# Performance work log

Measured on AMD Instinct MI355X. Metric: run time of the kernel, lower is better.

The kernel has to match this reference:

```python
import jax, jax.numpy as jnp
import numpy as np


def setup_inputs() -> dict:
    key = jax.random.key(0)
    k1, k2, k3 = jax.random.split(key, 3)
    n_nodes, d = 1_000_000, 128
    B, L, w, neg_size = 1024, 80, 5, 4
    A = L - w + 1  # 76 anchors per walk
    walk = jax.random.randint(k1, (B, L), 0, n_nodes)
    # torch.randint(low=1, high=n_nodes-1) -> values in [1, n_nodes-2]
    neg = jax.random.randint(k2, (B, A, neg_size), 1, n_nodes - 1)
    embed = jax.random.normal(k3, (n_nodes, d), dtype=jnp.float32)
    return {"walk": walk, "neg": neg, "embed": embed}


def reference(walk, neg, embed):
    B, L = walk.shape
    A = neg.shape[1]          # L - window_size + 1
    w = L - A + 1             # window_size
    anc = walk[:, :A]                                       # [B, A]
    # pos[b, t, i] = walk[b, t + 1 + i], i in [0, w-2]
    sl = jnp.arange(A)[:, None] + jnp.arange(1, w)[None, :]  # [A, w-1]
    pos = walk[:, sl]                                        # [B, A, w-1]
    e_anc = embed[anc]                                       # [B, A, D]
    # fused gather + per-window dot products
    pos_logit = jnp.einsum('bacd,bad->bac', embed[pos], e_anc)  # [B, A, w-1]
    neg_logit = jnp.einsum('bacd,bad->bac', embed[neg], e_anc)  # [B, A, neg]
    # BCEWithLogitsLoss with labels 1 (pos) and 0 (neg), mean over all elements:
    #   label=1 -> softplus(-x);  label=0 -> softplus(x)
    total = pos_logit.size + neg_logit.size
    loss = (jnp.sum(jax.nn.softplus(-pos_logit)) +
            jnp.sum(jax.nn.softplus(neg_logit))) / total
    return loss
```

## Files before the change

### kernel.cpp

```cpp
#include <hip/hip_runtime.h>
#include <math.h>

#define BD   1024
#define LW   80
#define AA   76
#define NEGS 4
#define D    128
#define PAIRS (BD * AA)
#define WAVES_PER_BLOCK 4
#define PAIRS_PER_WAVE 19
#define NBLOCKS BD

__device__ __forceinline__ float softplus(float x) {
    return fmaxf(x, 0.0f) + log1pf(__expf(-fabsf(x)));
}

__global__ __launch_bounds__(256, 4) void sg_partial(
    const int* __restrict__ walk, const int* __restrict__ neg,
    const float* __restrict__ embed, float* __restrict__ ws)
{
    __shared__ float s_wsum[WAVES_PER_BLOCK];
    const int tid  = threadIdx.x;
    const int lane = tid & 63;
    const int wave = __builtin_amdgcn_readfirstlane(tid >> 6);
    const int b    = blockIdx.x;
    const int a0   = wave * PAIRS_PER_WAVE;

    const float* erow = embed + (size_t)(lane * 2);
    const int*   wrow = walk + b * LW + a0;
    const int*   nrow = neg + (size_t)(b * AA + a0) * NEGS;

    float2 r[5];
    #pragma unroll
    for (int j = 0; j < 5; ++j)
        r[j] = *(const float2*)(erow + (size_t)wrow[j] * D);

    const bool hi1 = lane & 1;
    const bool hi2 = lane & 2;
    const bool hi3 = lane & 4;

    float wsum = 0.0f;

    #pragma unroll
    for (int i = 0; i < PAIRS_PER_WAVE; ++i) {
        const int4 nv = *(const int4*)(nrow + i * NEGS);
        const float2 e4 = *(const float2*)(erow + (size_t)nv.x * D);
        const float2 e5 = *(const float2*)(erow + (size_t)nv.y * D);
        const float2 e6 = *(const float2*)(erow + (size_t)nv.z * D);
        const float2 e7 = *(const float2*)(erow + (size_t)nv.w * D);

        const float2 ea = r[0];
        float a0v = fmaf(ea.x, r[1].x, ea.y * r[1].y);
        float a1v = fmaf(ea.x, r[2].x, ea.y * r[2].y);
        float a2v = fmaf(ea.x, r[3].x, ea.y * r[3].y);
        float a3v = fmaf(ea.x, r[4].x, ea.y * r[4].y);
        float a4v = fmaf(ea.x, e4.x,  ea.y * e4.y);
        float a5v = fmaf(ea.x, e5.x,  ea.y * e5.y);
        float a6v = fmaf(ea.x, e6.x,  ea.y * e6.y);
        float a7v = fmaf(ea.x, e7.x,  ea.y * e7.y);

        float b0 = (hi1 ? a4v : a0v) + __shfl_xor(hi1 ? a0v : a4v, 1);
        float b1 = (hi1 ? a5v : a1v) + __shfl_xor(hi1 ? a1v : a5v, 1);
        float b2 = (hi1 ? a6v : a2v) + __shfl_xor(hi1 ? a2v : a6v, 1);
        float b3 = (hi1 ? a7v : a3v) + __shfl_xor(hi1 ? a3v : a7v, 1);

        float c0 = (hi2 ? b2 : b0) + __shfl_xor(hi2 ? b0 : b2, 2);
        float c1 = (hi2 ? b3 : b1) + __shfl_xor(hi2 ? b1 : b3, 2);

        float dv = (hi3 ? c1 : c0) + __shfl_xor(hi3 ? c0 : c1, 4);
        dv += __shfl_xor(dv, 8);
        dv += __shfl_xor(dv, 16);
        dv += __shfl_xor(dv, 32);
        wsum += softplus(hi1 ? dv : -dv);

        if (i < PAIRS_PER_WAVE - 1) {
            #pragma unroll
            for (int j = 0; j < 4; ++j) r[j] = r[j + 1];
            r[4] = *(const float2*)(erow + (size_t)wrow[i + 5] * D);
        }
    }

    #pragma unroll
    for (int m = 1; m < 64; m <<= 1) wsum += __shfl_xor(wsum, m);

    if (lane == 0) s_wsum[wave] = wsum * 0.125f;
    __syncthreads();
    if (tid == 0)
        ws[blockIdx.x] = s_wsum[0] + s_wsum[1] + s_wsum[2] + s_wsum[3];
}

__global__ __launch_bounds__(256) void sg_reduce(
    const float* __restrict__ ws, float* __restrict__ out)
{
    __shared__ float s[4];
    const int tid = threadIdx.x;
    float sum = 0.0f;
    #pragma unroll
    for (int i = 0; i < NBLOCKS / 256; ++i) sum += ws[tid + i * 256];
    #pragma unroll
    for (int m = 1; m < 64; m <<= 1) sum += __shfl_xor(sum, m);
    const int wave = tid >> 6;
    const int lane = tid & 63;
    if (lane == 0) s[wave] = sum;
    __syncthreads();
    if (tid == 0) {
        const float total = (float)((size_t)PAIRS * 8);
        out[0] = (s[0] + s[1] + s[2] + s[3]) * (1.0f / total);
    }
}

extern "C" void kernel_launch(void* const* d_in, const int* in_sizes, int n_in,
                              void* d_out, int out_size, void* d_ws, size_t ws_size,
                              hipStream_t stream) {
    const int*   walk  = (const int*)d_in[0];
    const int*   neg   = (const int*)d_in[1];
    const float* embed = (const float*)d_in[2];
    float* ws  = (float*)d_ws;
    float* out = (float*)d_out;

    sg_partial<<<NBLOCKS, 256, 0, stream>>>(walk, neg, embed, ws);
    sg_reduce<<<1, 256, 0, stream>>>(ws, out);
}
```

Before: 587.4 us.

## Process two anchor pairs per wave with half-wave float4 row loads

Each half of the wave now handles a different anchor pair, with each lane loading float4 (16 bytes) instead of float2. This halves the number of gather instructions per row and removes the final cross-half shuffle from the dot-product reduction. The loop now runs nine double steps plus a tail for the odd 19th pair, and next-step rows are prefetched one iteration ahead. The cost is extra select and swap shuffles to give each half its anchor vector, more register pressure, and a duplicated tail path whose scaling must stay correct.

```diff
diff --git a/kernel.cpp b/kernel.cpp
--- a/kernel.cpp
+++ b/kernel.cpp
@@ -15,6 +15,29 @@
     return fmaxf(x, 0.0f) + log1pf(__expf(-fabsf(x)));
 }
 
+__device__ __forceinline__ float dot4(float4 a, float4 b) {
+    return fmaf(a.x, b.x, fmaf(a.y, b.y, fmaf(a.z, b.z, a.w * b.w)));
+}
+
+__device__ __forceinline__ float4 sel4(bool c, float4 a, float4 b) {
+    float4 r;
+    r.x = c ? a.x : b.x;  r.y = c ? a.y : b.y;
+    r.z = c ? a.z : b.z;  r.w = c ? a.w : b.w;
+    return r;
+}
+
+__device__ __forceinline__ float4 swap32(float4 v) {
+    float4 r;
+    r.x = __shfl_xor(v.x, 32);  r.y = __shfl_xor(v.y, 32);
+    r.z = __shfl_xor(v.z, 32);  r.w = __shfl_xor(v.w, 32);
+    return r;
+}
+
+__device__ __forceinline__ float4 pload(const float* ebase, bool half, int i0, int i1) {
+    const int idx = half ? i1 : i0;
+    return *(const float4*)(ebase + (size_t)idx * D);
+}
+
 __global__ __launch_bounds__(256, 4) void sg_partial(
     const int* __restrict__ walk, const int* __restrict__ neg,
     const float* __restrict__ embed, float* __restrict__ ws)
@@ -22,42 +45,68 @@
     __shared__ float s_wsum[WAVES_PER_BLOCK];
     const int tid  = threadIdx.x;
     const int lane = tid & 63;
+    const int l32  = lane & 31;
+    const bool half = lane >= 32;
     const int wave = __builtin_amdgcn_readfirstlane(tid >> 6);
     const int b    = blockIdx.x;
     const int a0   = wave * PAIRS_PER_WAVE;
 
-    const float* erow = embed + (size_t)(lane * 2);
-    const int*   wrow = walk + b * LW + a0;
-    const int*   nrow = neg + (size_t)(b * AA + a0) * NEGS;
+    const float* ebase = embed + l32 * 4;
+    const int*   wrow  = walk + b * LW + a0;
+    const int*   nrow  = neg + (size_t)(b * AA + a0) * NEGS;
 
-    float2 r[5];
-    #pragma unroll
-    for (int j = 0; j < 5; ++j)
-        r[j] = *(const float2*)(erow + (size_t)wrow[j] * D);
+    float4 w01 = pload(ebase, half, wrow[0], wrow[1]);
+    float4 w23 = pload(ebase, half, wrow[2], wrow[3]);
+    float4 w45 = pload(ebase, half, wrow[4], wrow[5]);
+
+    int4 nva = *(const int4*)(nrow);
+    int4 nvb = *(const int4*)(nrow + 4);
+    float4 n01 = pload(ebase, half, nva.x, nva.y);
+    float4 n23 = pload(ebase, half, nva.z, nva.w);
+    float4 n45 = pload(ebase, half, nvb.x, nvb.y);
+    float4 n67 = pload(ebase, half, nvb.z, nvb.w);
 
     const bool hi1 = lane & 1;
     const bool hi2 = lane & 2;
     const bool hi3 = lane & 4;
 
     float wsum = 0.0f;
+    float tsum = 0.0f;
 
     #pragma unroll
-    for (int i = 0; i < PAIRS_PER_WAVE; ++i) {
-        const int4 nv = *(const int4*)(nrow + i * NEGS);
-        const float2 e4 = *(const float2*)(erow + (size_t)nv.x * D);
-        const float2 e5 = *(const float2*)(erow + (size_t)nv.y * D);
-        const float2 e6 = *(const float2*)(erow + (size_t)nv.z * D);
-        const float2 e7 = *(const float2*)(erow + (size_t)nv.w * D);
+    for (int d = 0; d < 9; ++d) {
+        float4 nw, m01, m23, m45, m67;
+        if (d < 8) {
+            nw = pload(ebase, half, wrow[2*d + 6], wrow[2*d + 7]);
+            const int4 pa = *(const int4*)(nrow + 8*(d + 1));
+            const int4 pb = *(const int4*)(nrow + 8*(d + 1) + 4);
+            m01 = pload(ebase, half, pa.x, pa.y);
+            m23 = pload(ebase, half, pa.z, pa.w);
+            m45 = pload(ebase, half, pb.x, pb.y);
+            m67 = pload(ebase, half, pb.z, pb.w);
+        } else {
+            const int i22 = wrow[22];
+            nw = pload(ebase, half, i22, i22);
+            const int4 pa = *(const int4*)(nrow + 72);
+            m01 = pload(ebase, half, pa.x, pa.y);
+            m23 = pload(ebase, half, pa.z, pa.w);
+            m45 = m01;  m67 = m23;
+        }
 
-        const float2 ea = r[0];
-        float a0v = fmaf(ea.x, r[1].x, ea.y * r[1].y);
-        float a1v = fmaf(ea.x, r[2].x, ea.y * r[2].y);
-        float a2v = fmaf(ea.x, r[3].x, ea.y * r[3].y);
-        float a3v = fmaf(ea.x, r[4].x, ea.y * r[4].y);
-        float a4v = fmaf(ea.x, e4.x,  ea.y * e4.y);
-        float a5v = fmaf(ea.x, e5.x,  ea.y * e5.y);
-        float a6v = fmaf(ea.x, e6.x,  ea.y * e6.y);
-        float a7v = fmaf(ea.x, e7.x,  ea.y * e7.y);
+        const float4 Y   = swap32(w01);
+        const float4 Z0  = sel4(half, Y, w01);
+        const float4 Z1  = sel4(half, w01, Y);
+        const float4 Aop = sel4(half, w01, w23);
+        const float4 Bop = sel4(half, w23, w45);
+
+        const float a0v = dot4(Z0, Aop);
+        const float a1v = dot4(Z0, Bop);
+        const float a2v = dot4(Z1, w23);
+        const float a3v = dot4(Z1, w45);
+        const float a4v = dot4(Z0, n01);
+        const float a5v = dot4(Z0, n23);
+        const float a6v = dot4(Z1, n45);
+        const float a7v = dot4(Z1, n67);
 
         float b0 = (hi1 ? a4v : a0v) + __shfl_xor(hi1 ? a0v : a4v, 1);
         float b1 = (hi1 ? a5v : a1v) + __shfl_xor(hi1 ? a1v : a5v, 1);
@@ -70,20 +119,37 @@
         float dv = (hi3 ? c1 : c0) + __shfl_xor(hi3 ? c0 : c1, 4);
         dv += __shfl_xor(dv, 8);
         dv += __shfl_xor(dv, 16);
-        dv += __shfl_xor(dv, 32);
         wsum += softplus(hi1 ? dv : -dv);
 
-        if (i < PAIRS_PER_WAVE - 1) {
-            #pragma unroll
-            for (int j = 0; j < 4; ++j) r[j] = r[j + 1];
-            r[4] = *(const float2*)(erow + (size_t)wrow[i + 5] * D);
-        }
+        w01 = w23;  w23 = w45;  w45 = nw;
+        n01 = m01;  n23 = m23;  n45 = m45;  n67 = m67;
     }
 
+    {
+        const float4 Y   = swap32(w01);
+        const float4 Z0  = sel4(half, Y, w01);
+        const float4 Aop = sel4(half, w01, w23);
+        const float4 Bop = sel4(half, w23, w45);
+
+        const float t0 = dot4(Z0, Aop);
+        const float t1 = dot4(Z0, Bop);
+        const float t2 = dot4(Z0, n01);
+        const float t3 = dot4(Z0, n23);
+
+        float u0 = (hi1 ? t2 : t0) + __shfl_xor(hi1 ? t0 : t2, 1);
+        float u1 = (hi1 ? t3 : t1) + __shfl_xor(hi1 ? t1 : t3, 1);
+        float v  = (hi2 ? u1 : u0) + __shfl_xor(hi2 ? u0 : u1, 2);
+        v += __shfl_xor(v, 4);
+        v += __shfl_xor(v, 8);
+        v += __shfl_xor(v, 16);
+        tsum = softplus(hi1 ? v : -v);
+    }
+
+    float tot = wsum + 0.5f * tsum;
     #pragma unroll
-    for (int m = 1; m < 64; m <<= 1) wsum += __shfl_xor(wsum, m);
+    for (int m = 1; m < 64; m <<= 1) tot += __shfl_xor(tot, m);
 
-    if (lane == 0) s_wsum[wave] = wsum * 0.125f;
+    if (lane == 0) s_wsum[wave] = tot * 0.25f;
     __syncthreads();
     if (tid == 0)
         ws[blockIdx.x] = s_wsum[0] + s_wsum[1] + s_wsum[2] + s_wsum[3];
```

Measured after the change: 586.5 us. Within noise of the previous version (-0.2%).
